# Performance work log

Measured on AMD Instinct MI355X. Metric: run time of the kernel, lower is better.

Reference implementation:

```python
import jax, jax.numpy as jnp
import numpy as np

SCALE = 64.0
MARGIN = 0.35
EPS = 1e-12  # torch F.normalize eps


def _l2norm(a, axis):
    n = jnp.sqrt(jnp.sum(a * a, axis=axis, keepdims=True))
    return a / jnp.maximum(n, EPS)


def setup_inputs() -> dict:
    key = jax.random.key(0)
    k1, k2, k3 = jax.random.split(key, 3)
    B, D, C = 512, 512, 100000
    x = jax.random.normal(k1, (B, D), dtype=jnp.float32)
    gt = jax.random.randint(k2, (B,), 0, C, dtype=jnp.int64)
    # kaiming_normal_ on [C, D]: std = sqrt(2 / fan_in) with fan_in = D
    wt = jax.random.normal(k3, (C, D), dtype=jnp.float32) * np.sqrt(2.0 / D)
    return {"x": x, "gt": gt, "wt": wt}


def reference(x, gt, wt):
    wt_norm = _l2norm(wt, axis=1)          # [C, D]
    x_norm = _l2norm(x, axis=1)            # [B, D]
    cos = jnp.einsum("bd,cd->bc", x_norm, wt_norm)  # [B, C]
    # margin only at target index (avoids materializing one-hot)
    b = jnp.arange(x.shape[0])
    margin_score = cos.at[b, gt].add(-MARGIN)
    logits = SCALE * margin_score
    logp = jax.nn.log_softmax(logits, axis=-1)
    nll = -logp[b, gt]
    return jnp.mean(nll)
```

## Files before the change

kernel.cpp:

```cpp
#include <hip/hip_runtime.h>
#include <hip/hip_bf16.h>

#define DIM 512
#define BATCH 512
#define CCLS 100000
#define BM 256
#define BN 128
#define NT 782

typedef __attribute__((ext_vector_type(4))) float f32x4;

__device__ __forceinline__ void async_copy16(const unsigned char* g, unsigned char* l) {
  __builtin_amdgcn_global_load_lds((const __attribute__((address_space(1))) void*)g,
                                   (__attribute__((address_space(3))) void*)l, 16, 0, 0);
}

__global__ __launch_bounds__(256) void rownorm_fp8(const float* __restrict__ wt,
                                                   const float* __restrict__ x,
                                                   unsigned char* __restrict__ wn,
                                                   unsigned char* __restrict__ xn) {
  int wave = threadIdx.x >> 6;
  int lane = threadIdx.x & 63;
  int row4 = blockIdx.x * 4 + wave;
  const float* in;
  unsigned char* out;
  int row;
  if (row4 < CCLS) { in = wt; out = wn; row = row4; }
  else             { in = x;  out = xn; row = row4 - CCLS; }
  const float4* src = (const float4*)(in + (size_t)row * DIM);
  float4 v0 = src[2 * lane];
  float4 v1 = src[2 * lane + 1];
  float ss = v0.x*v0.x + v0.y*v0.y + v0.z*v0.z + v0.w*v0.w
           + v1.x*v1.x + v1.y*v1.y + v1.z*v1.z + v1.w*v1.w;
  #pragma unroll
  for (int off = 32; off > 0; off >>= 1) ss += __shfl_xor(ss, off, 64);
  float r = 1.0f / fmaxf(sqrtf(ss), 1e-12f);
  int p0 = __builtin_amdgcn_cvt_pk_fp8_f32(v0.x * r, v0.y * r, 0, false);
  p0     = __builtin_amdgcn_cvt_pk_fp8_f32(v0.z * r, v0.w * r, p0, true);
  int p1 = __builtin_amdgcn_cvt_pk_fp8_f32(v1.x * r, v1.y * r, 0, false);
  p1     = __builtin_amdgcn_cvt_pk_fp8_f32(v1.z * r, v1.w * r, p1, true);
  ((int2*)(out + (size_t)row * DIM))[lane] = make_int2(p0, p1);
}

__global__ __launch_bounds__(512, 4) void cosface_gemm(
    const unsigned char* __restrict__ xn,
    const unsigned char* __restrict__ wn,
    const int* __restrict__ gt,
    float* __restrict__ partial,
    float* __restrict__ tgt) {
  __shared__ __align__(16) unsigned char lds_a[BM * 128];
  __shared__ __align__(16) unsigned char lds_b[BN * 128];
  __shared__ float lds_rowsum[BM];
  __shared__ int lds_gt[BM];

  const int tid = threadIdx.x;
  const int lane = tid & 63;
  const int w = tid >> 6;
  const int wm = w >> 1;
  const int wn_ = w & 1;
  const int mt = blockIdx.x;
  const int nt = blockIdx.y;

  if (tid < BM) {
    lds_rowsum[tid] = 0.f;
    lds_gt[tid] = gt[mt * BM + tid];
  }

  const unsigned char* ga[4];
  const unsigned char* gb[2];
  #pragma unroll
  for (int j = 0; j < 4; ++j) {
    int c = j * 512 + tid;
    int m = c >> 3;
    int qg = (c & 7) ^ (m & 7);
    ga[j] = xn + (size_t)(mt * BM + m) * DIM + qg * 16;
  }
  #pragma unroll
  for (int j = 0; j < 2; ++j) {
    int c = j * 512 + tid;
    int m = c >> 3;
    int qg = (c & 7) ^ (m & 7);
    int rowB = nt * BN + m;
    if (rowB >= CCLS) rowB = CCLS - 1;
    gb[j] = wn + (size_t)rowB * DIM + qg * 16;
  }

  f32x4 acc[4][4];
  #pragma unroll
  for (int i = 0; i < 4; ++i)
    #pragma unroll
    for (int j = 0; j < 4; ++j)
      acc[i][j] = (f32x4){0.f, 0.f, 0.f, 0.f};

  const int quad = lane >> 4;
  const int l15 = lane & 15;
  const int arow = wm * 64 + l15;
  const int brow = wn_ * 64 + l15;
  const int swA = arow & 7;
  const int swB = brow & 7;

  for (int kk = 0; kk < 4; ++kk) {
    #pragma unroll
    for (int j = 0; j < 4; ++j)
      async_copy16(ga[j] + kk * 128, &lds_a[(j * 512 + w * 64) * 16]);
    #pragma unroll
    for (int j = 0; j < 2; ++j)
      async_copy16(gb[j] + kk * 128, &lds_b[(j * 512 + w * 64) * 16]);
    __syncthreads();
    #pragma unroll
    for (int s = 0; s < 4; ++s) {
      int g = s * 4 + quad;
      int cs = g >> 1;
      int h = (g & 1) * 8;
      long long af[4], bf[4];
      #pragma unroll
      for (int i = 0; i < 4; ++i) {
        af[i] = *(const long long*)&lds_a[(arow + i * 16) * 128 + ((cs ^ swA) * 16) + h];
        bf[i] = *(const long long*)&lds_b[(brow + i * 16) * 128 + ((cs ^ swB) * 16) + h];
      }
      #pragma unroll
      for (int i = 0; i < 4; ++i)
        #pragma unroll
        for (int j = 0; j < 4; ++j)
          acc[i][j] = __builtin_amdgcn_mfma_f32_16x16x32_fp8_fp8(af[i], bf[j], acc[i][j], 0, 0, 0);
    }
    __syncthreads();
  }

  #pragma unroll
  for (int i = 0; i < 4; ++i) {
    #pragma unroll
    for (int reg = 0; reg < 4; ++reg) {
      int m_loc = wm * 64 + i * 16 + quad * 4 + reg;
      int m_g = mt * BM + m_loc;
      int gtm = lds_gt[m_loc];
      float s = 0.f;
      #pragma unroll
      for (int j = 0; j < 4; ++j) {
        int n_g = nt * BN + wn_ * 64 + j * 16 + l15;
        float logit = 64.f * acc[i][j][reg];
        if (n_g == gtm) {
          logit -= 64.f * 0.35f;
          tgt[m_g] = logit;
        }
        if (n_g < CCLS) s += __expf(logit - 64.f);
      }
      #pragma unroll
      for (int off = 1; off < 16; off <<= 1) s += __shfl_xor(s, off, 64);
      if (l15 == 0) atomicAdd(&lds_rowsum[m_loc], s);
    }
  }
  __syncthreads();
  if (tid < BM)
    partial[(size_t)(mt * BM + tid) * NT + nt] = lds_rowsum[tid];
}

__global__ __launch_bounds__(64) void nll_rows(const float* __restrict__ partial,
                                               const float* __restrict__ tgt,
                                               float* __restrict__ nll) {
  int m = blockIdx.x;
  int lane = threadIdx.x;
  const float* row = partial + (size_t)m * NT;
  float s = 0.f;
  for (int t = lane; t < NT; t += 64) s += row[t];
  #pragma unroll
  for (int off = 32; off > 0; off >>= 1) s += __shfl_xor(s, off, 64);
  if (lane == 0) nll[m] = (logf(s) + 64.f) - tgt[m];
}

__global__ __launch_bounds__(512) void reduce_mean(const float* __restrict__ nll,
                                                   float* __restrict__ out) {
  __shared__ float red[BATCH];
  int m = threadIdx.x;
  red[m] = nll[m];
  __syncthreads();
  for (int k = 256; k > 0; k >>= 1) {
    if (m < k) red[m] += red[m + k];
    __syncthreads();
  }
  if (m == 0) out[0] = red[0] * (1.0f / BATCH);
}

extern "C" void kernel_launch(void* const* d_in, const int* in_sizes, int n_in,
                              void* d_out, int out_size, void* d_ws, size_t ws_size,
                              hipStream_t stream) {
  const float* x  = (const float*)d_in[0];
  const int*   gt = (const int*)d_in[1];
  const float* wt = (const float*)d_in[2];
  float* out = (float*)d_out;

  char* ws = (char*)d_ws;
  unsigned char* wn = (unsigned char*)ws;
  unsigned char* xn = (unsigned char*)(ws + 51200000);
  float* partial    = (float*)(ws + 51462144);
  float* tgt        = (float*)(ws + 53063680);
  float* nll        = (float*)(ws + 53065728);

  rownorm_fp8<<<(CCLS + BATCH) / 4, 256, 0, stream>>>(wt, x, wn, xn);
  cosface_gemm<<<dim3(2, NT), 512, 0, stream>>>(xn, wn, gt, partial, tgt);
  nll_rows<<<BATCH, 64, 0, stream>>>(partial, tgt, nll);
  reduce_mean<<<1, BATCH, 0, stream>>>(nll, out);
}
```

Baseline: 349.7 us.

## Fuse weight normalization and FP8 quantization into GEMM, apply norms post-accumulation

```diff
diff --git a/kernel.cpp b/kernel.cpp
--- a/kernel.cpp
+++ b/kernel.cpp
@@ -4,7 +4,6 @@
 #define DIM 512
 #define BATCH 512
 #define CCLS 100000
-#define BM 256
 #define BN 128
 #define NT 782
 
@@ -15,133 +14,155 @@
                                    (__attribute__((address_space(3))) void*)l, 16, 0, 0);
 }
 
-__global__ __launch_bounds__(256) void rownorm_fp8(const float* __restrict__ wt,
-                                                   const float* __restrict__ x,
-                                                   unsigned char* __restrict__ wn,
-                                                   unsigned char* __restrict__ xn) {
+__global__ __launch_bounds__(256) void xquant(const float* __restrict__ x,
+                                              unsigned char* __restrict__ xq,
+                                              float* __restrict__ nx) {
   int wave = threadIdx.x >> 6;
   int lane = threadIdx.x & 63;
-  int row4 = blockIdx.x * 4 + wave;
-  const float* in;
-  unsigned char* out;
-  int row;
-  if (row4 < CCLS) { in = wt; out = wn; row = row4; }
-  else             { in = x;  out = xn; row = row4 - CCLS; }
-  const float4* src = (const float4*)(in + (size_t)row * DIM);
+  int row = blockIdx.x * 4 + wave;
+  const float4* src = (const float4*)(x + (size_t)row * DIM);
   float4 v0 = src[2 * lane];
   float4 v1 = src[2 * lane + 1];
   float ss = v0.x*v0.x + v0.y*v0.y + v0.z*v0.z + v0.w*v0.w
            + v1.x*v1.x + v1.y*v1.y + v1.z*v1.z + v1.w*v1.w;
   #pragma unroll
   for (int off = 32; off > 0; off >>= 1) ss += __shfl_xor(ss, off, 64);
-  float r = 1.0f / fmaxf(sqrtf(ss), 1e-12f);
-  int p0 = __builtin_amdgcn_cvt_pk_fp8_f32(v0.x * r, v0.y * r, 0, false);
-  p0     = __builtin_amdgcn_cvt_pk_fp8_f32(v0.z * r, v0.w * r, p0, true);
-  int p1 = __builtin_amdgcn_cvt_pk_fp8_f32(v1.x * r, v1.y * r, 0, false);
-  p1     = __builtin_amdgcn_cvt_pk_fp8_f32(v1.z * r, v1.w * r, p1, true);
-  ((int2*)(out + (size_t)row * DIM))[lane] = make_int2(p0, p1);
-}
-
-__global__ __launch_bounds__(512, 4) void cosface_gemm(
-    const unsigned char* __restrict__ xn,
-    const unsigned char* __restrict__ wn,
+  int p0 = __builtin_amdgcn_cvt_pk_fp8_f32(v0.x, v0.y, 0, false);
+  p0     = __builtin_amdgcn_cvt_pk_fp8_f32(v0.z, v0.w, p0, true);
+  int p1 = __builtin_amdgcn_cvt_pk_fp8_f32(v1.x, v1.y, 0, false);
+  p1     = __builtin_amdgcn_cvt_pk_fp8_f32(v1.z, v1.w, p1, true);
+  ((int2*)(xq + (size_t)row * DIM))[lane] = make_int2(p0, p1);
+  if (lane == 0) nx[row] = fmaxf(sqrtf(ss), 1e-12f);
+}
+
+__global__ __launch_bounds__(1024) void cosface_fused(
+    const unsigned char* __restrict__ xq,
+    const float* __restrict__ wt,
     const int* __restrict__ gt,
+    const float* __restrict__ nx,
     float* __restrict__ partial,
     float* __restrict__ tgt) {
-  __shared__ __align__(16) unsigned char lds_a[BM * 128];
+  __shared__ __align__(16) unsigned char lds_a[512 * 128];
   __shared__ __align__(16) unsigned char lds_b[BN * 128];
-  __shared__ float lds_rowsum[BM];
-  __shared__ int lds_gt[BM];
+  __shared__ float lds_rowsum[BATCH];
+  __shared__ float lds_nx[BATCH];
+  __shared__ float lds_nw[BN];
+  __shared__ int lds_gt[BATCH];
 
   const int tid = threadIdx.x;
   const int lane = tid & 63;
   const int w = tid >> 6;
-  const int wm = w >> 1;
-  const int wn_ = w & 1;
-  const int mt = blockIdx.x;
-  const int nt = blockIdx.y;
-
-  if (tid < BM) {
+  const int wm = w >> 2;
+  const int wn_ = w & 3;
+  const int nt = blockIdx.x;
+
+  if (tid < BATCH) {
     lds_rowsum[tid] = 0.f;
-    lds_gt[tid] = gt[mt * BM + tid];
-  }
-
-  const unsigned char* ga[4];
-  const unsigned char* gb[2];
+    lds_gt[tid] = gt[tid];
+    lds_nx[tid] = nx[tid];
+  }
+  if (tid < BN) lds_nw[tid] = 0.f;
+
+  unsigned int oa[4];
   #pragma unroll
   for (int j = 0; j < 4; ++j) {
-    int c = j * 512 + tid;
+    int c = j * 1024 + tid;
     int m = c >> 3;
     int qg = (c & 7) ^ (m & 7);
-    ga[j] = xn + (size_t)(mt * BM + m) * DIM + qg * 16;
-  }
-  #pragma unroll
-  for (int j = 0; j < 2; ++j) {
-    int c = j * 512 + tid;
-    int m = c >> 3;
-    int qg = (c & 7) ^ (m & 7);
-    int rowB = nt * BN + m;
-    if (rowB >= CCLS) rowB = CCLS - 1;
-    gb[j] = wn + (size_t)rowB * DIM + qg * 16;
-  }
-
-  f32x4 acc[4][4];
-  #pragma unroll
-  for (int i = 0; i < 4; ++i)
-    #pragma unroll
-    for (int j = 0; j < 4; ++j)
+    oa[j] = (unsigned int)m * DIM + qg * 16;
+  }
+  const int mB = tid >> 3;
+  const int qgB = (tid & 7) ^ (mB & 7);
+  int rowB = nt * BN + mB;
+  if (rowB >= CCLS) rowB = CCLS - 1;
+  const float* wsrc = wt + (size_t)rowB * DIM + qgB * 16;
+
+  f32x4 acc[8][2];
+  #pragma unroll
+  for (int i = 0; i < 8; ++i)
+    #pragma unroll
+    for (int j = 0; j < 2; ++j)
       acc[i][j] = (f32x4){0.f, 0.f, 0.f, 0.f};
 
   const int quad = lane >> 4;
   const int l15 = lane & 15;
-  const int arow = wm * 64 + l15;
-  const int brow = wn_ * 64 + l15;
-  const int swA = arow & 7;
-  const int swB = brow & 7;
+  const int sw = l15 & 7;
+  __syncthreads();
 
   for (int kk = 0; kk < 4; ++kk) {
     #pragma unroll
     for (int j = 0; j < 4; ++j)
-      async_copy16(ga[j] + kk * 128, &lds_a[(j * 512 + w * 64) * 16]);
-    #pragma unroll
-    for (int j = 0; j < 2; ++j)
-      async_copy16(gb[j] + kk * 128, &lds_b[(j * 512 + w * 64) * 16]);
+      async_copy16(xq + oa[j] + kk * 128, &lds_a[(j * 1024 + w * 64) * 16]);
+    {
+      const float* p = wsrc + kk * 128;
+      float4 f0 = *(const float4*)(p);
+      float4 f1 = *(const float4*)(p + 4);
+      float4 f2 = *(const float4*)(p + 8);
+      float4 f3 = *(const float4*)(p + 12);
+      f0.x*=16.f; f0.y*=16.f; f0.z*=16.f; f0.w*=16.f;
+      f1.x*=16.f; f1.y*=16.f; f1.z*=16.f; f1.w*=16.f;
+      f2.x*=16.f; f2.y*=16.f; f2.z*=16.f; f2.w*=16.f;
+      f3.x*=16.f; f3.y*=16.f; f3.z*=16.f; f3.w*=16.f;
+      float ss = f0.x*f0.x + f0.y*f0.y + f0.z*f0.z + f0.w*f0.w
+               + f1.x*f1.x + f1.y*f1.y + f1.z*f1.z + f1.w*f1.w
+               + f2.x*f2.x + f2.y*f2.y + f2.z*f2.z + f2.w*f2.w
+               + f3.x*f3.x + f3.y*f3.y + f3.z*f3.z + f3.w*f3.w;
+      int p0 = __builtin_amdgcn_cvt_pk_fp8_f32(f0.x, f0.y, 0, false);
+      p0     = __builtin_amdgcn_cvt_pk_fp8_f32(f0.z, f0.w, p0, true);
+      int p1 = __builtin_amdgcn_cvt_pk_fp8_f32(f1.x, f1.y, 0, false);
+      p1     = __builtin_amdgcn_cvt_pk_fp8_f32(f1.z, f1.w, p1, true);
+      int p2 = __builtin_amdgcn_cvt_pk_fp8_f32(f2.x, f2.y, 0, false);
+      p2     = __builtin_amdgcn_cvt_pk_fp8_f32(f2.z, f2.w, p2, true);
+      int p3 = __builtin_amdgcn_cvt_pk_fp8_f32(f3.x, f3.y, 0, false);
+      p3     = __builtin_amdgcn_cvt_pk_fp8_f32(f3.z, f3.w, p3, true);
+      ((int4*)lds_b)[tid] = make_int4(p0, p1, p2, p3);
+      ss += __shfl_xor(ss, 1, 64);
+      ss += __shfl_xor(ss, 2, 64);
+      ss += __shfl_xor(ss, 4, 64);
+      if ((lane & 7) == 0) atomicAdd(&lds_nw[mB], ss);
+    }
     __syncthreads();
+
     #pragma unroll
     for (int s = 0; s < 4; ++s) {
       int g = s * 4 + quad;
       int cs = g >> 1;
       int h = (g & 1) * 8;
-      long long af[4], bf[4];
-      #pragma unroll
-      for (int i = 0; i < 4; ++i) {
-        af[i] = *(const long long*)&lds_a[(arow + i * 16) * 128 + ((cs ^ swA) * 16) + h];
-        bf[i] = *(const long long*)&lds_b[(brow + i * 16) * 128 + ((cs ^ swB) * 16) + h];
-      }
-      #pragma unroll
-      for (int i = 0; i < 4; ++i)
+      long long af[8], bf[2];
+      #pragma unroll
+      for (int i = 0; i < 8; ++i)
+        af[i] = *(const long long*)&lds_a[(wm * 128 + i * 16 + l15) * 128 + ((cs ^ sw) * 16) + h];
+      #pragma unroll
+      for (int j = 0; j < 2; ++j)
+        bf[j] = *(const long long*)&lds_b[(wn_ * 32 + j * 16 + l15) * 128 + ((cs ^ sw) * 16) + h];
+      #pragma unroll
+      for (int i = 0; i < 8; ++i)
         #pragma unroll
-        for (int j = 0; j < 4; ++j)
+        for (int j = 0; j < 2; ++j)
           acc[i][j] = __builtin_amdgcn_mfma_f32_16x16x32_fp8_fp8(af[i], bf[j], acc[i][j], 0, 0, 0);
     }
     __syncthreads();
   }
 
-  #pragma unroll
-  for (int i = 0; i < 4; ++i) {
+  float rnw[2];
+  #pragma unroll
+  for (int j = 0; j < 2; ++j)
+    rnw[j] = 1.0f / fmaxf(sqrtf(lds_nw[wn_ * 32 + j * 16 + l15]), 1e-12f);
+  #pragma unroll
+  for (int i = 0; i < 8; ++i) {
     #pragma unroll
     for (int reg = 0; reg < 4; ++reg) {
-      int m_loc = wm * 64 + i * 16 + quad * 4 + reg;
-      int m_g = mt * BM + m_loc;
+      int m_loc = wm * 128 + i * 16 + quad * 4 + reg;
       int gtm = lds_gt[m_loc];
+      float rx = 64.0f / lds_nx[m_loc];
       float s = 0.f;
       #pragma unroll
-      for (int j = 0; j < 4; ++j) {
-        int n_g = nt * BN + wn_ * 64 + j * 16 + l15;
-        float logit = 64.f * acc[i][j][reg];
+      for (int j = 0; j < 2; ++j) {
+        int n_g = nt * BN + wn_ * 32 + j * 16 + l15;
+        float logit = acc[i][j][reg] * rnw[j] * rx;
         if (n_g == gtm) {
           logit -= 64.f * 0.35f;
-          tgt[m_g] = logit;
+          tgt[m_loc] = logit;
         }
         if (n_g < CCLS) s += __expf(logit - 64.f);
       }
@@ -151,8 +172,8 @@
     }
   }
   __syncthreads();
-  if (tid < BM)
-    partial[(size_t)(mt * BM + tid) * NT + nt] = lds_rowsum[tid];
+  if (tid < BATCH)
+    partial[(size_t)tid * NT + nt] = lds_rowsum[tid];
 }
 
 __global__ __launch_bounds__(64) void nll_rows(const float* __restrict__ partial,
@@ -190,14 +211,14 @@
   float* out = (float*)d_out;
 
   char* ws = (char*)d_ws;
-  unsigned char* wn = (unsigned char*)ws;
-  unsigned char* xn = (unsigned char*)(ws + 51200000);
-  float* partial    = (float*)(ws + 51462144);
-  float* tgt        = (float*)(ws + 53063680);
-  float* nll        = (float*)(ws + 53065728);
-
-  rownorm_fp8<<<(CCLS + BATCH) / 4, 256, 0, stream>>>(wt, x, wn, xn);
-  cosface_gemm<<<dim3(2, NT), 512, 0, stream>>>(xn, wn, gt, partial, tgt);
+  unsigned char* xq = (unsigned char*)ws;
+  float* nx         = (float*)(ws + 262144);
+  float* partial    = (float*)(ws + 264192);
+  float* tgt        = (float*)(ws + 1865728);
+  float* nll        = (float*)(ws + 1867776);
+
+  xquant<<<BATCH / 4, 256, 0, stream>>>(x, xq, nx);
+  cosface_fused<<<NT, 1024, 0, stream>>>(xq, wt, gt, nx, partial, tgt);
   nll_rows<<<BATCH, 64, 0, stream>>>(partial, tgt, nll);
   reduce_mean<<<1, BATCH, 0, stream>>>(nll, out);
 }
```

New measurement: 393.7 us. +12.6%, slower.

## Double-buffer GEMM K-loop with 64-byte stages and XCD-aware block remap

Applied to the files above, without the earlier changes.

```diff
diff --git a/kernel.cpp b/kernel.cpp
--- a/kernel.cpp
+++ b/kernel.cpp
@@ -48,8 +48,8 @@
     const int* __restrict__ gt,
     float* __restrict__ partial,
     float* __restrict__ tgt) {
-  __shared__ __align__(16) unsigned char lds_a[BM * 128];
-  __shared__ __align__(16) unsigned char lds_b[BN * 128];
+  __shared__ __align__(16) unsigned char lds_a[2][BM * 64];
+  __shared__ __align__(16) unsigned char lds_b[2][BN * 64];
   __shared__ float lds_rowsum[BM];
   __shared__ int lds_gt[BM];
 
@@ -58,32 +58,42 @@
   const int w = tid >> 6;
   const int wm = w >> 1;
   const int wn_ = w & 1;
-  const int mt = blockIdx.x;
-  const int nt = blockIdx.y;
+
+  int orig = blockIdx.x;
+  int xcd = orig & 7;
+  int f = (xcd < 4 ? xcd * 196 : 4 * 196 + (xcd - 4) * 195) + (orig >> 3);
+  const int mt = f & 1;
+  const int nt = f >> 1;
 
   if (tid < BM) {
     lds_rowsum[tid] = 0.f;
     lds_gt[tid] = gt[mt * BM + tid];
   }
 
-  const unsigned char* ga[4];
-  const unsigned char* gb[2];
-  #pragma unroll
-  for (int j = 0; j < 4; ++j) {
-    int c = j * 512 + tid;
-    int m = c >> 3;
-    int qg = (c & 7) ^ (m & 7);
-    ga[j] = xn + (size_t)(mt * BM + m) * DIM + qg * 16;
-  }
+  unsigned int oa[2];
+  unsigned int ob;
   #pragma unroll
   for (int j = 0; j < 2; ++j) {
     int c = j * 512 + tid;
-    int m = c >> 3;
-    int qg = (c & 7) ^ (m & 7);
+    int m = c >> 2;
+    int qg = (c & 3) ^ (m & 3);
+    oa[j] = (unsigned int)(mt * BM + m) * DIM + qg * 16;
+  }
+  {
+    int m = tid >> 2;
+    int qg = (tid & 3) ^ (m & 3);
     int rowB = nt * BN + m;
     if (rowB >= CCLS) rowB = CCLS - 1;
-    gb[j] = wn + (size_t)rowB * DIM + qg * 16;
-  }
+    ob = (unsigned int)rowB * DIM + qg * 16;
+  }
+
+#define STAGE(sel, kk) do {                                                  \
+    _Pragma("unroll")                                                        \
+    for (int j = 0; j < 2; ++j)                                              \
+      async_copy16(xn + oa[j] + (kk) * 64,                                   \
+                   &lds_a[sel][(j * 512 + tid) * 16]);                       \
+    async_copy16(wn + ob + (kk) * 64, &lds_b[sel][tid * 16]);                \
+  } while (0)
 
   f32x4 acc[4][4];
   #pragma unroll
@@ -94,38 +104,42 @@
 
   const int quad = lane >> 4;
   const int l15 = lane & 15;
-  const int arow = wm * 64 + l15;
-  const int brow = wn_ * 64 + l15;
-  const int swA = arow & 7;
-  const int swB = brow & 7;
-
-  for (int kk = 0; kk < 4; ++kk) {
+  const int sw = l15 & 3;
+  const int csbase = quad >> 1;
+  const int h = (quad & 1) * 8;
+
+  STAGE(0, 0);
+  __syncthreads();
+
+  #pragma unroll
+  for (int kk = 0; kk < 8; ++kk) {
+    const int cur = kk & 1;
+    if (kk < 7) STAGE(cur ^ 1, kk + 1);
+
     #pragma unroll
-    for (int j = 0; j < 4; ++j)
-      async_copy16(ga[j] + kk * 128, &lds_a[(j * 512 + w * 64) * 16]);
-    #pragma unroll
-    for (int j = 0; j < 2; ++j)
-      async_copy16(gb[j] + kk * 128, &lds_b[(j * 512 + w * 64) * 16]);
-    __syncthreads();
-    #pragma unroll
-    for (int s = 0; s < 4; ++s) {
-      int g = s * 4 + quad;
-      int cs = g >> 1;
-      int h = (g & 1) * 8;
+    for (int s = 0; s < 2; ++s) {
+      int cs = s * 2 + csbase;
       long long af[4], bf[4];
       #pragma unroll
-      for (int i = 0; i < 4; ++i) {
-        af[i] = *(const long long*)&lds_a[(arow + i * 16) * 128 + ((cs ^ swA) * 16) + h];
-        bf[i] = *(const long long*)&lds_b[(brow + i * 16) * 128 + ((cs ^ swB) * 16) + h];
-      }
+      for (int i = 0; i < 4; ++i)
+        af[i] = *(const long long*)&lds_a[cur][(wm * 64 + i * 16 + l15) * 64 + ((cs ^ sw) * 16) + h];
+      #pragma unroll
+      for (int j = 0; j < 4; ++j)
+        bf[j] = *(const long long*)&lds_b[cur][(wn_ * 64 + j * 16 + l15) * 64 + ((cs ^ sw) * 16) + h];
       #pragma unroll
       for (int i = 0; i < 4; ++i)
         #pragma unroll
         for (int j = 0; j < 4; ++j)
           acc[i][j] = __builtin_amdgcn_mfma_f32_16x16x32_fp8_fp8(af[i], bf[j], acc[i][j], 0, 0, 0);
     }
-    __syncthreads();
-  }
+
+    if (kk < 7) {
+      asm volatile("s_waitcnt vmcnt(0)" ::: "memory");
+      __builtin_amdgcn_s_barrier();
+      asm volatile("" ::: "memory");
+    }
+  }
+#undef STAGE
 
   #pragma unroll
   for (int i = 0; i < 4; ++i) {
@@ -197,7 +211,7 @@
   float* nll        = (float*)(ws + 53065728);
 
   rownorm_fp8<<<(CCLS + BATCH) / 4, 256, 0, stream>>>(wt, x, wn, xn);
-  cosface_gemm<<<dim3(2, NT), 512, 0, stream>>>(xn, wn, gt, partial, tgt);
+  cosface_gemm<<<2 * NT, 512, 0, stream>>>(xn, wn, gt, partial, tgt);
   nll_rows<<<BATCH, 64, 0, stream>>>(partial, tgt, nll);
   reduce_mean<<<1, BATCH, 0, stream>>>(nll, out);
 }
```

Result: slower. 368.3 us (+5.3%).
